# Kernel optimization log

Hardware: AMD Instinct MI355X
Metric: run time of the kernel (lower is better)

The kernel has to match this reference:

```python
import jax, jax.numpy as jnp
import numpy as np

N_NODES = 200000
N_EDGES = 3200000
N_GRAPHS = 64
IN_DIM, HIDDEN, OUT_DIM = 128, 16, 64


def setup_inputs() -> dict:
    key = jax.random.key(0)
    ks = jax.random.split(key, 5)
    x = jax.random.normal(ks[0], (N_NODES, IN_DIM), dtype=jnp.float32)
    edge_index = jax.random.randint(ks[1], (2, N_EDGES), 0, N_NODES, dtype=jnp.int64)
    batch = jnp.sort(jax.random.randint(ks[2], (N_NODES,), 0, N_GRAPHS, dtype=jnp.int64))
    W1 = jax.random.normal(ks[3], (IN_DIM, HIDDEN), dtype=jnp.float32) * (1.0 / np.sqrt(IN_DIM))
    W2 = jax.random.normal(ks[4], (HIDDEN, OUT_DIM), dtype=jnp.float32) * (1.0 / np.sqrt(HIDDEN))
    b1 = jnp.zeros((HIDDEN,), jnp.float32)
    b2 = jnp.zeros((OUT_DIM,), jnp.float32)
    return {"x": x, "edge_index": edge_index, "batch": batch,
            "W1": W1, "b1": b1, "W2": W2, "b2": b2, "training": 0}


def _gcn_conv(x, W, b, row, col, n_nodes):
    # PyG GCNConv: add-self-loop symmetric normalization, transform then
    # gather-from-row / scatter-add-to-col.  (row, col) already include self-loops.
    h = x @ W                                             # [N, out]
    deg = jnp.zeros((n_nodes,), h.dtype).at[col].add(1.0)  # degree incl. self-loop (>=1)
    dinv = deg ** -0.5
    norm = dinv[row] * dinv[col]                          # [E+N]
    out = jnp.zeros((n_nodes, W.shape[1]), h.dtype).at[col].add(h[row] * norm[:, None])
    return out + b


def reference(x, edge_index, batch, W1, b1, W2, b2, training):
    n = x.shape[0]
    loops = jnp.arange(n, dtype=edge_index.dtype)
    row = jnp.concatenate([edge_index[0], loops])
    col = jnp.concatenate([edge_index[1], loops])
    h = _gcn_conv(x, W1, b1, row, col, n)
    h = jax.nn.relu(h)
    # F.dropout with training=False is identity (reference is deterministic)
    h = _gcn_conv(h, W2, b2, row, col, n)
    # per-graph sum pooling: replaces the Python torch.where loop
    graph_embeds = jax.ops.segment_sum(h, batch, num_segments=N_GRAPHS)
    return graph_embeds
```

## Files before the change

### kernel.cpp

```cpp
#include <hip/hip_runtime.h>


#define TPB 256
#define CHUNK 4096
#define BK_SHIFT 9
#define NPB 512
#define W1S 20

__device__ __forceinline__ float bf2f(unsigned short u) {
    union { unsigned int i; float f; } v; v.i = ((unsigned int)u) << 16; return v.f;
}
__device__ __forceinline__ unsigned short f2bf(float f) {
    union { float f; unsigned int i; } v; v.f = f;
    unsigned int r = v.i + 0x7fff + ((v.i >> 16) & 1);
    return (unsigned short)(r >> 16);
}
__device__ __forceinline__ void bfacc8(uint4 v, unsigned int m, float* a) {
    union { unsigned int i; float f; } lo, hi;
    v.x &= m; v.y &= m; v.z &= m; v.w &= m;
    lo.i = v.x << 16; hi.i = v.x & 0xffff0000u; a[0] += lo.f; a[1] += hi.f;
    lo.i = v.y << 16; hi.i = v.y & 0xffff0000u; a[2] += lo.f; a[3] += hi.f;
    lo.i = v.z << 16; hi.i = v.z & 0xffff0000u; a[4] += lo.f; a[5] += hi.f;
    lo.i = v.w << 16; hi.i = v.w & 0xffff0000u; a[6] += lo.f; a[7] += hi.f;
}
__device__ __forceinline__ void bfunp8(uint4 v, float* a) {
    union { unsigned int i; float f; } lo, hi;
    lo.i = v.x << 16; hi.i = v.x & 0xffff0000u; a[0] = lo.f; a[1] = hi.f;
    lo.i = v.y << 16; hi.i = v.y & 0xffff0000u; a[2] = lo.f; a[3] = hi.f;
    lo.i = v.z << 16; hi.i = v.z & 0xffff0000u; a[4] = lo.f; a[5] = hi.f;
    lo.i = v.w << 16; hi.i = v.w & 0xffff0000u; a[6] = lo.f; a[7] = hi.f;
}

__global__ __launch_bounds__(TPB) void hist_kernel(const int* __restrict__ col,
                                                   int* __restrict__ counts,
                                                   int E, int nblk, int nbuck) {
    __shared__ int hist[512];
    int t = threadIdx.x;
    for (int i = t; i < nbuck; i += TPB) hist[i] = 0;
    __syncthreads();
    int e0 = blockIdx.x * CHUNK;
    for (int i = t; i < CHUNK; i += TPB) {
        int e = e0 + i;
        if (e < E) atomicAdd(&hist[col[e] >> BK_SHIFT], 1);
    }
    __syncthreads();
    for (int i = t; i < nbuck; i += TPB) counts[i * nblk + blockIdx.x] = hist[i];
}

__global__ __launch_bounds__(TPB) void scan1_kernel(const int* __restrict__ in,
                                                    int* __restrict__ out,
                                                    int* __restrict__ bsum, int L) {
    __shared__ int s[TPB];
    int t = threadIdx.x;
    int i = blockIdx.x * TPB + t;
    int d = (i < L) ? in[i] : 0;
    s[t] = d; __syncthreads();
    for (int off = 1; off < TPB; off <<= 1) {
        int v = (t >= off) ? s[t - off] : 0;
        __syncthreads();
        s[t] += v;
        __syncthreads();
    }
    if (i < L) out[i] = s[t] - d;
    if (t == TPB - 1) bsum[blockIdx.x] = s[t];
}

__global__ __launch_bounds__(1024) void scan2_kernel(int* __restrict__ bsum, int nb) {
    __shared__ int s[1024];
    int t = threadIdx.x;
    int i0 = t * 2, i1 = t * 2 + 1;
    int v0 = (i0 < nb) ? bsum[i0] : 0;
    int v1 = (i1 < nb) ? bsum[i1] : 0;
    int pv = v0 + v1;
    s[t] = pv; __syncthreads();
    for (int off = 1; off < 1024; off <<= 1) {
        int u = (t >= off) ? s[t - off] : 0;
        __syncthreads();
        s[t] += u;
        __syncthreads();
    }
    int exc = s[t] - pv;
    if (i0 < nb) bsum[i0] = exc;
    if (i1 < nb) bsum[i1] = exc + v0;
}

__device__ __forceinline__ int cbase_at(const int* counts, const int* bsum, int f) {
    return counts[f] + bsum[f >> 8];
}

__global__ __launch_bounds__(TPB) void scatter_kernel(
        const int* __restrict__ row, const int* __restrict__ col,
        const int* __restrict__ counts, const int* __restrict__ bsum,
        int E, int nblk, int nbuck,
        int* __restrict__ bucketed) {
    __shared__ int slhist[512];
    __shared__ int sgd[512];
    __shared__ unsigned short ssidx[CHUNK];
    __shared__ int swtot[4];
    int id = (int)blockIdx.x, t = threadIdx.x;
    int e0 = id * CHUNK;
    int nE = min(CHUNK, E - e0);
    int Ltot = nbuck * nblk;
    int lane = t & 63, w = t >> 6;
    int bk0 = 2 * t, bk1 = 2 * t + 1;
    int cb0 = 0, cb1 = 0, c0 = 0, c1 = 0;
    if (bk0 < nbuck) {
        int f = bk0 * nblk + id;
        cb0 = cbase_at(counts, bsum, f);
        int nx = (f + 1 < Ltot) ? cbase_at(counts, bsum, f + 1) : E;
        c0 = nx - cb0;
    }
    if (bk1 < nbuck) {
        int f = bk1 * nblk + id;
        cb1 = cbase_at(counts, bsum, f);
        int nx = (f + 1 < Ltot) ? cbase_at(counts, bsum, f + 1) : E;
        c1 = nx - cb1;
    }
    int s = c0 + c1;
    int v = s;
#pragma unroll
    for (int d = 1; d < 64; d <<= 1) {
        int u2 = __shfl_up(v, d, 64);
        if (lane >= d) v += u2;
    }
    if (lane == 63) swtot[w] = v;
    __syncthreads();
    int wbase = 0;
#pragma unroll
    for (int i = 0; i < 4; ++i) wbase += (i < w) ? swtot[i] : 0;
    int o0 = wbase + v - s;
    int o1 = o0 + c0;
    if (bk0 < nbuck) { slhist[bk0] = o0; sgd[bk0] = cb0 - o0; }
    if (bk1 < nbuck) { slhist[bk1] = o1; sgd[bk1] = cb1 - o1; }
    __syncthreads();
    for (int i = t; i < nE; i += TPB) {
        int c = col[e0 + i];
        int lp = atomicAdd(&slhist[c >> BK_SHIFT], 1);
        ssidx[lp] = (unsigned short)i;
    }
    __syncthreads();
    for (int j = t; j < nE; j += TPB) {
        int i = ssidx[j];
        int c = col[e0 + i];
        int r = row[e0 + i];
        bucketed[sgd[c >> BK_SHIFT] + j] = ((c & (NPB - 1)) << 18) | r;
    }
}

__global__ __launch_bounds__(TPB) void gemm_kernel(
        const float* __restrict__ x, const float* __restrict__ W1,
        unsigned short* __restrict__ h1b, int N) {
    __shared__ float w1s[128 * W1S];
    int t = threadIdx.x;
    for (int i = t; i < 128 * 16; i += TPB)
        w1s[(i >> 4) * W1S + (i & 15)] = W1[i];
    __syncthreads();
    int g = t >> 2, q = t & 3;
    int nA = (int)blockIdx.x * 128 + g;
    int nB = nA + 64;
    int nAc = min(nA, N - 1), nBc = min(nB, N - 1);
    const float4* xA = (const float4*)(x + (size_t)nAc * 128);
    const float4* xB = (const float4*)(x + (size_t)nBc * 128);
    float4 xvA[8], xvB[8];
#pragma unroll
    for (int i = 0; i < 8; ++i) xvA[i] = xA[i * 4 + q];
#pragma unroll
    for (int i = 0; i < 8; ++i) xvB[i] = xB[i * 4 + q];
    float accA[16], accB[16];
#pragma unroll
    for (int k = 0; k < 16; ++k) { accA[k] = 0.f; accB[k] = 0.f; }
#pragma unroll
    for (int i = 0; i < 8; ++i) {
        float xjA[4] = {xvA[i].x, xvA[i].y, xvA[i].z, xvA[i].w};
        float xjB[4] = {xvB[i].x, xvB[i].y, xvB[i].z, xvB[i].w};
#pragma unroll
        for (int j = 0; j < 4; ++j) {
            int k = i * 16 + q * 4 + j;
            const float4* w4 = (const float4*)&w1s[k * W1S];
            float4 wa = w4[0], wb = w4[1], wc = w4[2], wd = w4[3];
            float xa = xjA[j], xb = xjB[j];
            accA[0]  = fmaf(xa, wa.x, accA[0]);  accA[1]  = fmaf(xa, wa.y, accA[1]);
            accA[2]  = fmaf(xa, wa.z, accA[2]);  accA[3]  = fmaf(xa, wa.w, accA[3]);
            accA[4]  = fmaf(xa, wb.x, accA[4]);  accA[5]  = fmaf(xa, wb.y, accA[5]);
            accA[6]  = fmaf(xa, wb.z, accA[6]);  accA[7]  = fmaf(xa, wb.w, accA[7]);
            accA[8]  = fmaf(xa, wc.x, accA[8]);  accA[9]  = fmaf(xa, wc.y, accA[9]);
            accA[10] = fmaf(xa, wc.z, accA[10]); accA[11] = fmaf(xa, wc.w, accA[11]);
            accA[12] = fmaf(xa, wd.x, accA[12]); accA[13] = fmaf(xa, wd.y, accA[13]);
            accA[14] = fmaf(xa, wd.z, accA[14]); accA[15] = fmaf(xa, wd.w, accA[15]);
            accB[0]  = fmaf(xb, wa.x, accB[0]);  accB[1]  = fmaf(xb, wa.y, accB[1]);
            accB[2]  = fmaf(xb, wa.z, accB[2]);  accB[3]  = fmaf(xb, wa.w, accB[3]);
            accB[4]  = fmaf(xb, wb.x, accB[4]);  accB[5]  = fmaf(xb, wb.y, accB[5]);
            accB[6]  = fmaf(xb, wb.z, accB[6]);  accB[7]  = fmaf(xb, wb.w, accB[7]);
            accB[8]  = fmaf(xb, wc.x, accB[8]);  accB[9]  = fmaf(xb, wc.y, accB[9]);
            accB[10] = fmaf(xb, wc.z, accB[10]); accB[11] = fmaf(xb, wc.w, accB[11]);
            accB[12] = fmaf(xb, wd.x, accB[12]); accB[13] = fmaf(xb, wd.y, accB[13]);
            accB[14] = fmaf(xb, wd.z, accB[14]); accB[15] = fmaf(xb, wd.w, accB[15]);
        }
    }
#pragma unroll
    for (int d = 1; d < 4; d <<= 1) {
#pragma unroll
        for (int k = 0; k < 16; ++k) {
            accA[k] += __shfl_xor(accA[k], d, 4);
            accB[k] += __shfl_xor(accB[k], d, 4);
        }
    }
    if (nA < N) {
        unsigned int u0 = (unsigned int)f2bf(accA[4 * q]) |
                          ((unsigned int)f2bf(accA[4 * q + 1]) << 16);
        unsigned int u1 = (unsigned int)f2bf(accA[4 * q + 2]) |
                          ((unsigned int)f2bf(accA[4 * q + 3]) << 16);
        *(uint2*)&h1b[(size_t)nA * 16 + 4 * q] = make_uint2(u0, u1);
    }
    if (nB < N) {
        unsigned int u0 = (unsigned int)f2bf(accB[4 * q]) |
                          ((unsigned int)f2bf(accB[4 * q + 1]) << 16);
        unsigned int u1 = (unsigned int)f2bf(accB[4 * q + 2]) |
                          ((unsigned int)f2bf(accB[4 * q + 3]) << 16);
        *(uint2*)&h1b[(size_t)nB * 16 + 4 * q] = make_uint2(u0, u1);
    }
}

__global__ __launch_bounds__(TPB) void sort_kernel(
        const int* __restrict__ bucketed,
        const int* __restrict__ counts, const int* __restrict__ bsum,
        int E, int nblk, int nbuck,
        int* __restrict__ csr, int* __restrict__ offs, float* __restrict__ dinv,
        const unsigned short* __restrict__ h1b, unsigned short* __restrict__ h1p, int N) {
    __shared__ int lhist[NPB];
    __shared__ int part[TPB];
    __shared__ float sdinv[NPB];
    int bk = blockIdx.x, t = threadIdx.x;
    int n0 = bk << BK_SHIFT;
    int n1 = min(n0 + NPB, N);
    int e0 = cbase_at(counts, bsum, bk * nblk);
    int e1 = (bk + 1 < nbuck) ? cbase_at(counts, bsum, (bk + 1) * nblk) : E;

    lhist[t] = 0; lhist[t + TPB] = 0;
    __syncthreads();
    for (int i = e0 + t; i < e1; i += TPB)
        atomicAdd(&lhist[bucketed[i] >> 18], 1);
    __syncthreads();

    int base = t * 2;
    int c0 = lhist[base], c1 = lhist[base + 1];
    int s = c0 + c1;
    part[t] = s;
    __syncthreads();
    for (int off = 1; off < TPB; off <<= 1) {
        int v = (t >= off) ? part[t - off] : 0;
        __syncthreads();
        part[t] += v;
        __syncthreads();
    }
    int o0 = e0 + part[t] - s;
    int o1 = o0 + c0;
    lhist[base] = o0; lhist[base + 1] = o1;
    sdinv[base]     = rsqrtf((float)c0 + 1.0f);
    sdinv[base + 1] = rsqrtf((float)c1 + 1.0f);
    int n = n0 + base;
    if (n + 0 < N) { offs[n + 0] = o0; dinv[n + 0] = sdinv[base]; }
    if (n + 1 < N) { offs[n + 1] = o1; dinv[n + 1] = sdinv[base + 1]; }
    __syncthreads();

    for (int i = e0 + t; i < e1; i += TPB) {
        int v = bucketed[i];
        int pos = atomicAdd(&lhist[v >> 18], 1);
        csr[pos] = v & 0x3FFFF;
    }
    int nq = (n1 - n0) * 4;
    for (int i = t; i < nq; i += TPB) {
        float dv = sdinv[i >> 2];
        uint2 u = ((const uint2*)h1b)[(size_t)n0 * 4 + i];
        float f0 = bf2f((unsigned short)(u.x & 0xffff));
        float f1 = bf2f((unsigned short)(u.x >> 16));
        float f2 = bf2f((unsigned short)(u.y & 0xffff));
        float f3 = bf2f((unsigned short)(u.y >> 16));
        ((ushort4*)h1p)[(size_t)n0 * 4 + i] =
            make_ushort4(f2bf(f0 * dv), f2bf(f1 * dv), f2bf(f2 * dv), f2bf(f3 * dv));
    }
    if (bk == 0 && t == 0) offs[N] = E;
}

__global__ __launch_bounds__(TPB) void gather1_kernel(const int* __restrict__ csr,
                                                      const int* __restrict__ offs,
                                                      const unsigned short* __restrict__ h1p,
                                                      const float* __restrict__ dinv,
                                                      const float* __restrict__ b1,
                                                      unsigned short* __restrict__ h2p, int N) {
    int t = threadIdx.x;
    int c = blockIdx.x * 16 + (t >> 4);
    int l = t & 15;
    int half = l & 1;
    int sub  = l >> 1;
    if (c >= N) return;
    int p0 = offs[c], p1 = offs[c + 1];
    float a[8];
#pragma unroll
    for (int k = 0; k < 8; ++k) a[k] = 0.f;
    for (int p = p0; p < p1; p += 16) {
        int s16 = csr[min(p + l, p1 - 1)];
#pragma unroll
        for (int h = 0; h < 2; ++h) {
            int e = 8 * h + sub;
            int src = __shfl(s16, e, 16);
            unsigned int m = ((p + e) < p1) ? 0xffffffffu : 0u;
            uint4 v = *(const uint4*)&h1p[(size_t)src * 16 + 8 * half];
            bfacc8(v, m, a);
        }
    }
#pragma unroll
    for (int d = 2; d < 16; d <<= 1) {
#pragma unroll
        for (int k = 0; k < 8; ++k) a[k] += __shfl_xor(a[k], d, 16);
    }
    if (l < 2) {
        float dc = dinv[c];
        uint4 sv = *(const uint4*)&h1p[(size_t)c * 16 + 8 * l];
        float sf[8];
        bfunp8(sv, sf);
        unsigned int uo[4];
#pragma unroll
        for (int q = 0; q < 4; ++q) {
            float r0 = fmaf(dc, a[2 * q] + sf[2 * q], b1[8 * l + 2 * q]);
            float r1 = fmaf(dc, a[2 * q + 1] + sf[2 * q + 1], b1[8 * l + 2 * q + 1]);
            r0 = dc * fmaxf(r0, 0.f);
            r1 = dc * fmaxf(r1, 0.f);
            uo[q] = (unsigned int)f2bf(r0) | ((unsigned int)f2bf(r1) << 16);
        }
        *(uint4*)&h2p[(size_t)c * 16 + 8 * l] = make_uint4(uo[0], uo[1], uo[2], uo[3]);
    }
}

__global__ __launch_bounds__(TPB) void gather2f_kernel(
        const int* __restrict__ csr, const int* __restrict__ offs,
        const unsigned short* __restrict__ h2p, const float* __restrict__ dinv,
        const float* __restrict__ W2, const float* __restrict__ b2,
        const int* __restrict__ batch, float* __restrict__ out, int N) {
    __shared__ float w2s[16 * 64];
    __shared__ float asT[64 * 17];
    __shared__ float pool[64];
    int t = threadIdx.x;
    for (int i = t; i < 16 * 64; i += TPB) w2s[i] = W2[i];
    if (t < 64) pool[t] = 0.f;

    int n0 = blockIdx.x * 64;
    int nLast = min(n0 + 63, N - 1);
    int g0 = batch[n0];
    bool uniform = (batch[nLast] == g0);

    int grp = t >> 4, l = t & 15;
    int half = l & 1, sub = l >> 1;
#pragma unroll 1
    for (int it = 0; it < 4; ++it) {
        int m = grp * 4 + it;
        int c = n0 + m;
        if (c < N) {
            int p0 = offs[c], p1 = offs[c + 1];
            float a[8];
#pragma unroll
            for (int k = 0; k < 8; ++k) a[k] = 0.f;
            for (int p = p0; p < p1; p += 16) {
                int s16 = csr[min(p + l, p1 - 1)];
#pragma unroll
                for (int h = 0; h < 2; ++h) {
                    int e = 8 * h + sub;
                    int src = __shfl(s16, e, 16);
                    unsigned int mm = ((p + e) < p1) ? 0xffffffffu : 0u;
                    uint4 v = *(const uint4*)&h2p[(size_t)src * 16 + 8 * half];
                    bfacc8(v, mm, a);
                }
            }
#pragma unroll
            for (int d = 2; d < 16; d <<= 1) {
#pragma unroll
                for (int k = 0; k < 8; ++k) a[k] += __shfl_xor(a[k], d, 16);
            }
            if (l < 2) {
                float dc = dinv[c];
                uint4 sv = *(const uint4*)&h2p[(size_t)c * 16 + 8 * l];
                float sf[8];
                bfunp8(sv, sf);
#pragma unroll
                for (int k = 0; k < 8; ++k)
                    asT[m * 17 + 8 * l + k] = dc * (a[k] + sf[k]);
            }
        }
    }
    __syncthreads();

    int wave = t >> 6, j = t & 63;
    float w2reg[16];
#pragma unroll
    for (int kx = 0; kx < 16; ++kx) w2reg[kx] = w2s[kx * 64 + j];
    float b2j = b2[j];
    float val = 0.f;
    int g_cur = -1;
#pragma unroll 1
    for (int mi = 0; mi < 16; ++mi) {
        int m = wave * 16 + mi;
        int c = n0 + m;
        if (c >= N) break;
        const float* ar = &asT[m * 17];
        float y = b2j;
#pragma unroll
        for (int kx = 0; kx < 16; ++kx) y = fmaf(ar[kx], w2reg[kx], y);
        if (uniform) {
            val += y;
        } else {
            int g = batch[c];
            if (g != g_cur) {
                if (g_cur >= 0) atomicAdd(&out[(size_t)g_cur * 64 + j], val);
                val = 0.f;
                g_cur = g;
            }
            val += y;
        }
    }
    if (uniform) {
        atomicAdd(&pool[j], val);
        __syncthreads();
        if (t < 64) atomicAdd(&out[(size_t)g0 * 64 + t], pool[t]);
    } else {
        if (g_cur >= 0) atomicAdd(&out[(size_t)g_cur * 64 + j], val);
    }
}

static inline size_t align64(size_t v) { return (v + 63) & ~(size_t)63; }

extern "C" void kernel_launch(void* const* d_in, const int* in_sizes, int n_in,
                              void* d_out, int out_size, void* d_ws, size_t ws_size,
                              hipStream_t stream) {
    const float* x     = (const float*)d_in[0];
    const int*   ei    = (const int*)d_in[1];
    const int*   batch = (const int*)d_in[2];
    const float* W1    = (const float*)d_in[3];
    const float* b1    = (const float*)d_in[4];
    const float* W2    = (const float*)d_in[5];
    const float* b2    = (const float*)d_in[6];

    const int N = in_sizes[0] / 128;
    const int E = in_sizes[1] / 2;
    const int* row = ei;
    const int* col = ei + E;

    const int NBLK  = (E + CHUNK - 1) / CHUNK;
    const int NBUCK = (N + NPB - 1) / NPB;
    const int L     = NBUCK * NBLK;
    const int NBS   = (L + TPB - 1) / TPB;
    const int NG2   = (N + 127) / 128;

    char* p = (char*)d_ws;
    int*            counts   = (int*)p;            p += align64((size_t)L * 4);
    int*            bsum     = (int*)p;            p += align64(2048 * 4);
    int*            bucketed = (int*)p;            p += align64((size_t)E * 4);
    int*            csr      = (int*)p;            p += align64((size_t)E * 4);
    int*            offs     = (int*)p;            p += align64((size_t)(N + 1) * 4);
    float*          dinv     = (float*)p;          p += align64((size_t)N * 4);
    unsigned short* h1b      = (unsigned short*)p; p += align64((size_t)N * 16 * 2);
    unsigned short* h1p      = (unsigned short*)p; p += align64((size_t)N * 16 * 2);
    unsigned short* h2p      = (unsigned short*)p; p += align64((size_t)N * 16 * 2);
    float*          out      = (float*)d_out;

    hipMemsetAsync(out, 0, (size_t)out_size * sizeof(float), stream);

    hist_kernel<<<NBLK, TPB, 0, stream>>>(col, counts, E, NBLK, NBUCK);
    scan1_kernel<<<NBS, TPB, 0, stream>>>(counts, counts, bsum, L);
    scan2_kernel<<<1, 1024, 0, stream>>>(bsum, NBS);
    scatter_kernel<<<NBLK, TPB, 0, stream>>>(row, col, counts, bsum,
                                             E, NBLK, NBUCK, bucketed);
    gemm_kernel<<<NG2, TPB, 0, stream>>>(x, W1, h1b, N);
    sort_kernel<<<NBUCK, TPB, 0, stream>>>(bucketed, counts, bsum, E, NBLK, NBUCK,
                                           csr, offs, dinv, h1b, h1p, N);
    gather1_kernel<<<(N + 15) / 16, TPB, 0, stream>>>(csr, offs, h1p, dinv, b1, h2p, N);
    gather2f_kernel<<<(N + 63) / 64, TPB, 0, stream>>>(csr, offs, h2p, dinv,
                                                       W2, b2, batch, out, N);
}
```

Before: 344.0 us.

## Replace two-pass bucket sort CSR build with atomic-cursor scatter fused with GEMM

Replaces the bucketed two-level counting sort (hist, block-bucket scan, scatter, per-bucket sort) with a per-node degree histogram via global atomics, a scan over nodes, and a direct scatter into CSR using per-node atomic cursors. The CSR scatter blocks and the x@W1 GEMM blocks are interleaved in one launch so the memory-bound GEMM overlaps with the atomic scatter, and dinv scaling is folded into the GEMM epilogue, dropping the separate h1b buffer pass. This removes the intermediate bucketed array and a kernel, but relies on global atomics over 3.2M edges with random targets, and neighbour order within CSR rows becomes nondeterministic.

```diff
diff --git a/kernel.cpp b/kernel.cpp
--- a/kernel.cpp
+++ b/kernel.cpp
@@ -3,8 +3,6 @@
 
 #define TPB 256
 #define CHUNK 4096
-#define BK_SHIFT 9
-#define NPB 512
 #define W1S 20
 
 __device__ __forceinline__ float bf2f(unsigned short u) {
@@ -31,20 +29,14 @@
     lo.i = v.w << 16; hi.i = v.w & 0xffff0000u; a[6] = lo.f; a[7] = hi.f;
 }
 
-__global__ __launch_bounds__(TPB) void hist_kernel(const int* __restrict__ col,
-                                                   int* __restrict__ counts,
-                                                   int E, int nblk, int nbuck) {
-    __shared__ int hist[512];
-    int t = threadIdx.x;
-    for (int i = t; i < nbuck; i += TPB) hist[i] = 0;
-    __syncthreads();
-    int e0 = blockIdx.x * CHUNK;
-    for (int i = t; i < CHUNK; i += TPB) {
-        int e = e0 + i;
-        if (e < E) atomicAdd(&hist[col[e] >> BK_SHIFT], 1);
-    }
-    __syncthreads();
-    for (int i = t; i < nbuck; i += TPB) counts[i * nblk + blockIdx.x] = hist[i];
+__global__ __launch_bounds__(TPB) void deg_kernel(const int* __restrict__ col,
+                                                  int* __restrict__ deg, int E) {
+    int base = (int)blockIdx.x * (TPB * 8) + threadIdx.x;
+#pragma unroll
+    for (int k = 0; k < 8; ++k) {
+        int e = base + k * TPB;
+        if (e < E) atomicAdd(&deg[col[e]], 1);
+    }
 }
 
 __global__ __launch_bounds__(TPB) void scan1_kernel(const int* __restrict__ in,
@@ -84,79 +76,49 @@
     if (i1 < nb) bsum[i1] = exc + v0;
 }
 
-__device__ __forceinline__ int cbase_at(const int* counts, const int* bsum, int f) {
-    return counts[f] + bsum[f >> 8];
-}
-
-__global__ __launch_bounds__(TPB) void scatter_kernel(
+__global__ __launch_bounds__(TPB) void finalize_kernel(
+        const int* __restrict__ deg, const int* __restrict__ dscan,
+        const int* __restrict__ bsum,
+        int* __restrict__ offs, int* __restrict__ cursor,
+        float* __restrict__ dinv, int N, int E) {
+    int n = blockIdx.x * TPB + threadIdx.x;
+    if (n < N) {
+        int o = dscan[n] + bsum[n >> 8];
+        offs[n] = o;
+        cursor[n] = o;
+        dinv[n] = rsqrtf((float)deg[n] + 1.0f);
+    }
+    if (n == 0) offs[N] = E;
+}
+
+__global__ __launch_bounds__(TPB) void scatgemm_kernel(
         const int* __restrict__ row, const int* __restrict__ col,
-        const int* __restrict__ counts, const int* __restrict__ bsum,
-        int E, int nblk, int nbuck,
-        int* __restrict__ bucketed) {
-    __shared__ int slhist[512];
-    __shared__ int sgd[512];
-    __shared__ unsigned short ssidx[CHUNK];
-    __shared__ int swtot[4];
-    int id = (int)blockIdx.x, t = threadIdx.x;
-    int e0 = id * CHUNK;
-    int nE = min(CHUNK, E - e0);
-    int Ltot = nbuck * nblk;
-    int lane = t & 63, w = t >> 6;
-    int bk0 = 2 * t, bk1 = 2 * t + 1;
-    int cb0 = 0, cb1 = 0, c0 = 0, c1 = 0;
-    if (bk0 < nbuck) {
-        int f = bk0 * nblk + id;
-        cb0 = cbase_at(counts, bsum, f);
-        int nx = (f + 1 < Ltot) ? cbase_at(counts, bsum, f + 1) : E;
-        c0 = nx - cb0;
-    }
-    if (bk1 < nbuck) {
-        int f = bk1 * nblk + id;
-        cb1 = cbase_at(counts, bsum, f);
-        int nx = (f + 1 < Ltot) ? cbase_at(counts, bsum, f + 1) : E;
-        c1 = nx - cb1;
-    }
-    int s = c0 + c1;
-    int v = s;
-#pragma unroll
-    for (int d = 1; d < 64; d <<= 1) {
-        int u2 = __shfl_up(v, d, 64);
-        if (lane >= d) v += u2;
-    }
-    if (lane == 63) swtot[w] = v;
-    __syncthreads();
-    int wbase = 0;
-#pragma unroll
-    for (int i = 0; i < 4; ++i) wbase += (i < w) ? swtot[i] : 0;
-    int o0 = wbase + v - s;
-    int o1 = o0 + c0;
-    if (bk0 < nbuck) { slhist[bk0] = o0; sgd[bk0] = cb0 - o0; }
-    if (bk1 < nbuck) { slhist[bk1] = o1; sgd[bk1] = cb1 - o1; }
-    __syncthreads();
-    for (int i = t; i < nE; i += TPB) {
-        int c = col[e0 + i];
-        int lp = atomicAdd(&slhist[c >> BK_SHIFT], 1);
-        ssidx[lp] = (unsigned short)i;
-    }
-    __syncthreads();
-    for (int j = t; j < nE; j += TPB) {
-        int i = ssidx[j];
-        int c = col[e0 + i];
-        int r = row[e0 + i];
-        bucketed[sgd[c >> BK_SHIFT] + j] = ((c & (NPB - 1)) << 18) | r;
-    }
-}
-
-__global__ __launch_bounds__(TPB) void gemm_kernel(
+        int* __restrict__ cursor, int* __restrict__ csr, int E,
         const float* __restrict__ x, const float* __restrict__ W1,
-        unsigned short* __restrict__ h1b, int N) {
+        const float* __restrict__ dinv,
+        unsigned short* __restrict__ h1p, int N, int ns, int ng) {
     __shared__ float w1s[128 * W1S];
-    int t = threadIdx.x;
+    int b = (int)blockIdx.x, t = threadIdx.x;
+    int M = min(ns, ng);
+    int role, id;
+    if (b < 2 * M) { role = b & 1; id = b >> 1; }
+    else           { role = (ns > ng) ? 0 : 1; id = b - M; }
+
+    if (role == 0) {
+        int e0 = id * CHUNK;
+        int e1 = min(e0 + CHUNK, E);
+        for (int e = e0 + t; e < e1; e += TPB) {
+            int c = col[e];
+            int pos = atomicAdd(&cursor[c], 1);
+            csr[pos] = row[e];
+        }
+        return;
+    }
     for (int i = t; i < 128 * 16; i += TPB)
         w1s[(i >> 4) * W1S + (i & 15)] = W1[i];
     __syncthreads();
     int g = t >> 2, q = t & 3;
-    int nA = (int)blockIdx.x * 128 + g;
+    int nA = id * 128 + g;
     int nB = nA + 64;
     int nAc = min(nA, N - 1), nBc = min(nB, N - 1);
     const float4* xA = (const float4*)(x + (size_t)nAc * 128);
@@ -206,80 +168,21 @@
         }
     }
     if (nA < N) {
-        unsigned int u0 = (unsigned int)f2bf(accA[4 * q]) |
-                          ((unsigned int)f2bf(accA[4 * q + 1]) << 16);
-        unsigned int u1 = (unsigned int)f2bf(accA[4 * q + 2]) |
-                          ((unsigned int)f2bf(accA[4 * q + 3]) << 16);
-        *(uint2*)&h1b[(size_t)nA * 16 + 4 * q] = make_uint2(u0, u1);
+        float dA = dinv[nA];
+        unsigned int u0 = (unsigned int)f2bf(dA * accA[4 * q]) |
+                          ((unsigned int)f2bf(dA * accA[4 * q + 1]) << 16);
+        unsigned int u1 = (unsigned int)f2bf(dA * accA[4 * q + 2]) |
+                          ((unsigned int)f2bf(dA * accA[4 * q + 3]) << 16);
+        *(uint2*)&h1p[(size_t)nA * 16 + 4 * q] = make_uint2(u0, u1);
     }
     if (nB < N) {
-        unsigned int u0 = (unsigned int)f2bf(accB[4 * q]) |
-                          ((unsigned int)f2bf(accB[4 * q + 1]) << 16);
-        unsigned int u1 = (unsigned int)f2bf(accB[4 * q + 2]) |
-                          ((unsigned int)f2bf(accB[4 * q + 3]) << 16);
-        *(uint2*)&h1b[(size_t)nB * 16 + 4 * q] = make_uint2(u0, u1);
-    }
-}
-
-__global__ __launch_bounds__(TPB) void sort_kernel(
-        const int* __restrict__ bucketed,
-        const int* __restrict__ counts, const int* __restrict__ bsum,
-        int E, int nblk, int nbuck,
-        int* __restrict__ csr, int* __restrict__ offs, float* __restrict__ dinv,
-        const unsigned short* __restrict__ h1b, unsigned short* __restrict__ h1p, int N) {
-    __shared__ int lhist[NPB];
-    __shared__ int part[TPB];
-    __shared__ float sdinv[NPB];
-    int bk = blockIdx.x, t = threadIdx.x;
-    int n0 = bk << BK_SHIFT;
-    int n1 = min(n0 + NPB, N);
-    int e0 = cbase_at(counts, bsum, bk * nblk);
-    int e1 = (bk + 1 < nbuck) ? cbase_at(counts, bsum, (bk + 1) * nblk) : E;
-
-    lhist[t] = 0; lhist[t + TPB] = 0;
-    __syncthreads();
-    for (int i = e0 + t; i < e1; i += TPB)
-        atomicAdd(&lhist[bucketed[i] >> 18], 1);
-    __syncthreads();
-
-    int base = t * 2;
-    int c0 = lhist[base], c1 = lhist[base + 1];
-    int s = c0 + c1;
-    part[t] = s;
-    __syncthreads();
-    for (int off = 1; off < TPB; off <<= 1) {
-        int v = (t >= off) ? part[t - off] : 0;
-        __syncthreads();
-        part[t] += v;
-        __syncthreads();
-    }
-    int o0 = e0 + part[t] - s;
-    int o1 = o0 + c0;
-    lhist[base] = o0; lhist[base + 1] = o1;
-    sdinv[base]     = rsqrtf((float)c0 + 1.0f);
-    sdinv[base + 1] = rsqrtf((float)c1 + 1.0f);
-    int n = n0 + base;
-    if (n + 0 < N) { offs[n + 0] = o0; dinv[n + 0] = sdinv[base]; }
-    if (n + 1 < N) { offs[n + 1] = o1; dinv[n + 1] = sdinv[base + 1]; }
-    __syncthreads();
-
-    for (int i = e0 + t; i < e1; i += TPB) {
-        int v = bucketed[i];
-        int pos = atomicAdd(&lhist[v >> 18], 1);
-        csr[pos] = v & 0x3FFFF;
-    }
-    int nq = (n1 - n0) * 4;
-    for (int i = t; i < nq; i += TPB) {
-        float dv = sdinv[i >> 2];
-        uint2 u = ((const uint2*)h1b)[(size_t)n0 * 4 + i];
-        float f0 = bf2f((unsigned short)(u.x & 0xffff));
-        float f1 = bf2f((unsigned short)(u.x >> 16));
-        float f2 = bf2f((unsigned short)(u.y & 0xffff));
-        float f3 = bf2f((unsigned short)(u.y >> 16));
-        ((ushort4*)h1p)[(size_t)n0 * 4 + i] =
-            make_ushort4(f2bf(f0 * dv), f2bf(f1 * dv), f2bf(f2 * dv), f2bf(f3 * dv));
-    }
-    if (bk == 0 && t == 0) offs[N] = E;
+        float dB = dinv[nB];
+        unsigned int u0 = (unsigned int)f2bf(dB * accB[4 * q]) |
+                          ((unsigned int)f2bf(dB * accB[4 * q + 1]) << 16);
+        unsigned int u1 = (unsigned int)f2bf(dB * accB[4 * q + 2]) |
+                          ((unsigned int)f2bf(dB * accB[4 * q + 3]) << 16);
+        *(uint2*)&h1p[(size_t)nB * 16 + 4 * q] = make_uint2(u0, u1);
+    }
 }
 
 __global__ __launch_bounds__(TPB) void gather1_kernel(const int* __restrict__ csr,
@@ -444,34 +347,33 @@
     const int* row = ei;
     const int* col = ei + E;
 
-    const int NBLK  = (E + CHUNK - 1) / CHUNK;
-    const int NBUCK = (N + NPB - 1) / NPB;
-    const int L     = NBUCK * NBLK;
-    const int NBS   = (L + TPB - 1) / TPB;
-    const int NG2   = (N + 127) / 128;
+    const int NS   = (E + CHUNK - 1) / CHUNK;
+    const int NG   = (N + 127) / 128;
+    const int NBD  = (E + TPB * 8 - 1) / (TPB * 8);
+    const int NBN  = (N + TPB - 1) / TPB;
 
     char* p = (char*)d_ws;
-    int*            counts   = (int*)p;            p += align64((size_t)L * 4);
-    int*            bsum     = (int*)p;            p += align64(2048 * 4);
-    int*            bucketed = (int*)p;            p += align64((size_t)E * 4);
-    int*            csr      = (int*)p;            p += align64((size_t)E * 4);
-    int*            offs     = (int*)p;            p += align64((size_t)(N + 1) * 4);
-    float*          dinv     = (float*)p;          p += align64((size_t)N * 4);
-    unsigned short* h1b      = (unsigned short*)p; p += align64((size_t)N * 16 * 2);
-    unsigned short* h1p      = (unsigned short*)p; p += align64((size_t)N * 16 * 2);
-    unsigned short* h2p      = (unsigned short*)p; p += align64((size_t)N * 16 * 2);
-    float*          out      = (float*)d_out;
+    int*            deg    = (int*)p;            p += align64((size_t)N * 4);
+    int*            dscan  = (int*)p;            p += align64((size_t)N * 4);
+    int*            bsum   = (int*)p;            p += align64(2048 * 4);
+    int*            cursor = (int*)p;            p += align64((size_t)N * 4);
+    int*            csr    = (int*)p;            p += align64((size_t)E * 4);
+    int*            offs   = (int*)p;            p += align64((size_t)(N + 1) * 4);
+    float*          dinv   = (float*)p;          p += align64((size_t)N * 4);
+    unsigned short* h1p    = (unsigned short*)p; p += align64((size_t)N * 16 * 2);
+    unsigned short* h2p    = (unsigned short*)p; p += align64((size_t)N * 16 * 2);
+    float*          out    = (float*)d_out;
 
     hipMemsetAsync(out, 0, (size_t)out_size * sizeof(float), stream);
-
-    hist_kernel<<<NBLK, TPB, 0, stream>>>(col, counts, E, NBLK, NBUCK);
-    scan1_kernel<<<NBS, TPB, 0, stream>>>(counts, counts, bsum, L);
-    scan2_kernel<<<1, 1024, 0, stream>>>(bsum, NBS);
-    scatter_kernel<<<NBLK, TPB, 0, stream>>>(row, col, counts, bsum,
-                                             E, NBLK, NBUCK, bucketed);
-    gemm_kernel<<<NG2, TPB, 0, stream>>>(x, W1, h1b, N);
-    sort_kernel<<<NBUCK, TPB, 0, stream>>>(bucketed, counts, bsum, E, NBLK, NBUCK,
-                                           csr, offs, dinv, h1b, h1p, N);
+    hipMemsetAsync(deg, 0, (size_t)N * 4, stream);
+
+    deg_kernel<<<NBD, TPB, 0, stream>>>(col, deg, E);
+    scan1_kernel<<<NBN, TPB, 0, stream>>>(deg, dscan, bsum, N);
+    scan2_kernel<<<1, 1024, 0, stream>>>(bsum, NBN);
+    finalize_kernel<<<NBN, TPB, 0, stream>>>(deg, dscan, bsum, offs, cursor,
+                                             dinv, N, E);
+    scatgemm_kernel<<<NS + NG, TPB, 0, stream>>>(row, col, cursor, csr, E,
+                                                 x, W1, dinv, h1p, N, NS, NG);
     gather1_kernel<<<(N + 15) / 16, TPB, 0, stream>>>(csr, offs, h1p, dinv, b1, h2p, N);
     gather2f_kernel<<<(N + 63) / 64, TPB, 0, stream>>>(csr, offs, h2p, dinv,
                                                        W2, b2, batch, out, N);
```

New measurement: 590.8 us. 71.8% more time.

## Merge scatter and GEMM into one interleaved launch; widen gather to 32 edges

Applied to the files above, without the earlier changes.

The bucket-scatter kernel and the x@W1 GEMM kernel become one launch whose blocks alternate between the two roles, so the memory-bound scatter and the GEMM can run at the same time and one launch is saved. Shared memory is unioned between the roles, so the block's shared footprint is the larger of the two. The gather loops in both GCN layers now process 32 edges per iteration with four independent predicated loads instead of two masked loads. This raises memory-level parallelism at the cost of more registers and more wasted lanes on low-degree nodes.

```diff
diff --git a/kernel.cpp b/kernel.cpp
--- a/kernel.cpp
+++ b/kernel.cpp
@@ -15,9 +15,8 @@
     unsigned int r = v.i + 0x7fff + ((v.i >> 16) & 1);
     return (unsigned short)(r >> 16);
 }
-__device__ __forceinline__ void bfacc8(uint4 v, unsigned int m, float* a) {
+__device__ __forceinline__ void bfacc8(uint4 v, float* a) {
     union { unsigned int i; float f; } lo, hi;
-    v.x &= m; v.y &= m; v.z &= m; v.w &= m;
     lo.i = v.x << 16; hi.i = v.x & 0xffff0000u; a[0] += lo.f; a[1] += hi.f;
     lo.i = v.y << 16; hi.i = v.y & 0xffff0000u; a[2] += lo.f; a[3] += hi.f;
     lo.i = v.z << 16; hi.i = v.z & 0xffff0000u; a[4] += lo.f; a[5] += hi.f;
@@ -29,6 +28,30 @@
     lo.i = v.y << 16; hi.i = v.y & 0xffff0000u; a[2] = lo.f; a[3] = hi.f;
     lo.i = v.z << 16; hi.i = v.z & 0xffff0000u; a[4] = lo.f; a[5] = hi.f;
     lo.i = v.w << 16; hi.i = v.w & 0xffff0000u; a[6] = lo.f; a[7] = hi.f;
+}
+
+__device__ __forceinline__ void gather32(const int* __restrict__ csr,
+                                         const unsigned short* __restrict__ src_feat,
+                                         int p, int p1, int l, int half, int sub,
+                                         float* a) {
+    int s_lo = csr[min(p + l, p1 - 1)];
+    int s_hi = csr[min(p + 16 + l, p1 - 1)];
+    int rem = p1 - p;
+    int e0 = sub, e1 = 8 + sub, e2 = 16 + sub, e3 = 24 + sub;
+    int src0 = __shfl(s_lo, e0, 16);
+    int src1 = __shfl(s_lo, e1, 16);
+    int src2 = __shfl(s_hi, e2 - 16, 16);
+    int src3 = __shfl(s_hi, e3 - 16, 16);
+    uint4 u0 = make_uint4(0, 0, 0, 0), u1 = make_uint4(0, 0, 0, 0);
+    uint4 u2 = make_uint4(0, 0, 0, 0), u3 = make_uint4(0, 0, 0, 0);
+    if (e0 < rem) u0 = *(const uint4*)&src_feat[(size_t)src0 * 16 + 8 * half];
+    if (e1 < rem) u1 = *(const uint4*)&src_feat[(size_t)src1 * 16 + 8 * half];
+    if (e2 < rem) u2 = *(const uint4*)&src_feat[(size_t)src2 * 16 + 8 * half];
+    if (e3 < rem) u3 = *(const uint4*)&src_feat[(size_t)src3 * 16 + 8 * half];
+    bfacc8(u0, a);
+    bfacc8(u1, a);
+    bfacc8(u2, a);
+    bfacc8(u3, a);
 }
 
 __global__ __launch_bounds__(TPB) void hist_kernel(const int* __restrict__ col,
@@ -88,75 +111,81 @@
     return counts[f] + bsum[f >> 8];
 }
 
-__global__ __launch_bounds__(TPB) void scatter_kernel(
+__global__ __launch_bounds__(TPB) void s1c_gemm_kernel(
         const int* __restrict__ row, const int* __restrict__ col,
         const int* __restrict__ counts, const int* __restrict__ bsum,
         int E, int nblk, int nbuck,
-        int* __restrict__ bucketed) {
-    __shared__ int slhist[512];
-    __shared__ int sgd[512];
-    __shared__ unsigned short ssidx[CHUNK];
-    __shared__ int swtot[4];
-    int id = (int)blockIdx.x, t = threadIdx.x;
-    int e0 = id * CHUNK;
-    int nE = min(CHUNK, E - e0);
-    int Ltot = nbuck * nblk;
-    int lane = t & 63, w = t >> 6;
-    int bk0 = 2 * t, bk1 = 2 * t + 1;
-    int cb0 = 0, cb1 = 0, c0 = 0, c1 = 0;
-    if (bk0 < nbuck) {
-        int f = bk0 * nblk + id;
-        cb0 = cbase_at(counts, bsum, f);
-        int nx = (f + 1 < Ltot) ? cbase_at(counts, bsum, f + 1) : E;
-        c0 = nx - cb0;
-    }
-    if (bk1 < nbuck) {
-        int f = bk1 * nblk + id;
-        cb1 = cbase_at(counts, bsum, f);
-        int nx = (f + 1 < Ltot) ? cbase_at(counts, bsum, f + 1) : E;
-        c1 = nx - cb1;
-    }
-    int s = c0 + c1;
-    int v = s;
-#pragma unroll
-    for (int d = 1; d < 64; d <<= 1) {
-        int u2 = __shfl_up(v, d, 64);
-        if (lane >= d) v += u2;
-    }
-    if (lane == 63) swtot[w] = v;
-    __syncthreads();
-    int wbase = 0;
-#pragma unroll
-    for (int i = 0; i < 4; ++i) wbase += (i < w) ? swtot[i] : 0;
-    int o0 = wbase + v - s;
-    int o1 = o0 + c0;
-    if (bk0 < nbuck) { slhist[bk0] = o0; sgd[bk0] = cb0 - o0; }
-    if (bk1 < nbuck) { slhist[bk1] = o1; sgd[bk1] = cb1 - o1; }
-    __syncthreads();
-    for (int i = t; i < nE; i += TPB) {
-        int c = col[e0 + i];
-        int lp = atomicAdd(&slhist[c >> BK_SHIFT], 1);
-        ssidx[lp] = (unsigned short)i;
-    }
-    __syncthreads();
-    for (int j = t; j < nE; j += TPB) {
-        int i = ssidx[j];
-        int c = col[e0 + i];
-        int r = row[e0 + i];
-        bucketed[sgd[c >> BK_SHIFT] + j] = ((c & (NPB - 1)) << 18) | r;
-    }
-}
-
-__global__ __launch_bounds__(TPB) void gemm_kernel(
+        int* __restrict__ bucketed,
         const float* __restrict__ x, const float* __restrict__ W1,
-        unsigned short* __restrict__ h1b, int N) {
-    __shared__ float w1s[128 * W1S];
-    int t = threadIdx.x;
+        unsigned short* __restrict__ h1b, int N, int nbg) {
+    __shared__ __align__(16) char sbuf[2048 + 2048 + 8192 + 64];
+    int* slhist = (int*)sbuf;
+    int* sgd    = (int*)(sbuf + 2048);
+    unsigned short* ssidx = (unsigned short*)(sbuf + 4096);
+    int* swtot  = (int*)(sbuf + 4096 + 8192);
+    float* w1s  = (float*)sbuf;
+
+    int b = (int)blockIdx.x, t = threadIdx.x;
+    int M = min(nblk, nbg);
+    int role, id;
+    if (b < 2 * M) { role = b & 1; id = b >> 1; }
+    else           { role = (nblk > nbg) ? 0 : 1; id = b - M; }
+
+    if (role == 0) {
+        int e0 = id * CHUNK;
+        int nE = min(CHUNK, E - e0);
+        int Ltot = nbuck * nblk;
+        int lane = t & 63, w = t >> 6;
+        int bk0 = 2 * t, bk1 = 2 * t + 1;
+        int cb0 = 0, cb1 = 0, c0 = 0, c1 = 0;
+        if (bk0 < nbuck) {
+            int f = bk0 * nblk + id;
+            cb0 = cbase_at(counts, bsum, f);
+            int nx = (f + 1 < Ltot) ? cbase_at(counts, bsum, f + 1) : E;
+            c0 = nx - cb0;
+        }
+        if (bk1 < nbuck) {
+            int f = bk1 * nblk + id;
+            cb1 = cbase_at(counts, bsum, f);
+            int nx = (f + 1 < Ltot) ? cbase_at(counts, bsum, f + 1) : E;
+            c1 = nx - cb1;
+        }
+        int s = c0 + c1;
+        int v = s;
+#pragma unroll
+        for (int d = 1; d < 64; d <<= 1) {
+            int u2 = __shfl_up(v, d, 64);
+            if (lane >= d) v += u2;
+        }
+        if (lane == 63) swtot[w] = v;
+        __syncthreads();
+        int wbase = 0;
+#pragma unroll
+        for (int i = 0; i < 4; ++i) wbase += (i < w) ? swtot[i] : 0;
+        int o0 = wbase + v - s;
+        int o1 = o0 + c0;
+        if (bk0 < nbuck) { slhist[bk0] = o0; sgd[bk0] = cb0 - o0; }
+        if (bk1 < nbuck) { slhist[bk1] = o1; sgd[bk1] = cb1 - o1; }
+        __syncthreads();
+        for (int i = t; i < nE; i += TPB) {
+            int c = col[e0 + i];
+            int lp = atomicAdd(&slhist[c >> BK_SHIFT], 1);
+            ssidx[lp] = (unsigned short)i;
+        }
+        __syncthreads();
+        for (int j = t; j < nE; j += TPB) {
+            int i = ssidx[j];
+            int c = col[e0 + i];
+            int r = row[e0 + i];
+            bucketed[sgd[c >> BK_SHIFT] + j] = ((c & (NPB - 1)) << 18) | r;
+        }
+        return;
+    }
     for (int i = t; i < 128 * 16; i += TPB)
         w1s[(i >> 4) * W1S + (i & 15)] = W1[i];
     __syncthreads();
     int g = t >> 2, q = t & 3;
-    int nA = (int)blockIdx.x * 128 + g;
+    int nA = id * 128 + g;
     int nB = nA + 64;
     int nAc = min(nA, N - 1), nBc = min(nB, N - 1);
     const float4* xA = (const float4*)(x + (size_t)nAc * 128);
@@ -298,17 +327,8 @@
     float a[8];
 #pragma unroll
     for (int k = 0; k < 8; ++k) a[k] = 0.f;
-    for (int p = p0; p < p1; p += 16) {
-        int s16 = csr[min(p + l, p1 - 1)];
-#pragma unroll
-        for (int h = 0; h < 2; ++h) {
-            int e = 8 * h + sub;
-            int src = __shfl(s16, e, 16);
-            unsigned int m = ((p + e) < p1) ? 0xffffffffu : 0u;
-            uint4 v = *(const uint4*)&h1p[(size_t)src * 16 + 8 * half];
-            bfacc8(v, m, a);
-        }
-    }
+    for (int p = p0; p < p1; p += 32)
+        gather32(csr, h1p, p, p1, l, half, sub, a);
 #pragma unroll
     for (int d = 2; d < 16; d <<= 1) {
 #pragma unroll
@@ -360,17 +380,8 @@
             float a[8];
 #pragma unroll
             for (int k = 0; k < 8; ++k) a[k] = 0.f;
-            for (int p = p0; p < p1; p += 16) {
-                int s16 = csr[min(p + l, p1 - 1)];
-#pragma unroll
-                for (int h = 0; h < 2; ++h) {
-                    int e = 8 * h + sub;
-                    int src = __shfl(s16, e, 16);
-                    unsigned int mm = ((p + e) < p1) ? 0xffffffffu : 0u;
-                    uint4 v = *(const uint4*)&h2p[(size_t)src * 16 + 8 * half];
-                    bfacc8(v, mm, a);
-                }
-            }
+            for (int p = p0; p < p1; p += 32)
+                gather32(csr, h2p, p, p1, l, half, sub, a);
 #pragma unroll
             for (int d = 2; d < 16; d <<= 1) {
 #pragma unroll
@@ -448,7 +459,7 @@
     const int NBUCK = (N + NPB - 1) / NPB;
     const int L     = NBUCK * NBLK;
     const int NBS   = (L + TPB - 1) / TPB;
-    const int NG2   = (N + 127) / 128;
+    const int NBG   = (N + 127) / 128;
 
     char* p = (char*)d_ws;
     int*            counts   = (int*)p;            p += align64((size_t)L * 4);
@@ -467,9 +478,9 @@
     hist_kernel<<<NBLK, TPB, 0, stream>>>(col, counts, E, NBLK, NBUCK);
     scan1_kernel<<<NBS, TPB, 0, stream>>>(counts, counts, bsum, L);
     scan2_kernel<<<1, 1024, 0, stream>>>(bsum, NBS);
-    scatter_kernel<<<NBLK, TPB, 0, stream>>>(row, col, counts, bsum,
-                                             E, NBLK, NBUCK, bucketed);
-    gemm_kernel<<<NG2, TPB, 0, stream>>>(x, W1, h1b, N);
+    s1c_gemm_kernel<<<NBLK + NBG, TPB, 0, stream>>>(row, col, counts, bsum,
+                                                    E, NBLK, NBUCK,
+                                                    bucketed, x, W1, h1b, N, NBG);
     sort_kernel<<<NBUCK, TPB, 0, stream>>>(bucketed, counts, bsum, E, NBLK, NBUCK,
                                            csr, offs, dinv, h1b, h1p, N);
     gather1_kernel<<<(N + 15) / 16, TPB, 0, stream>>>(csr, offs, h1p, dinv, b1, h2p, N);
```

Measured after the change: 331.4 us. 3.7% less time.
